# Kernel tuning notes

Hardware: AMD Instinct MI355X
Metric: run time of the kernel (lower is better)

Reference implementation:

```python
import jax, jax.numpy as jnp
import numpy as np

N_HEAD = 16
D_MODEL = 1024
D_K = 64
D_V = 64
LN_EPS = 1e-6


def setup_inputs() -> dict:
    key = jax.random.key(0)
    ks = jax.random.split(key, 10)
    B, S = 2, 2048
    scale = 0.02
    return {
        "q": jax.random.normal(ks[0], (B, S, D_MODEL), jnp.float32),
        "k": jax.random.normal(ks[1], (B, S, D_MODEL), jnp.float32),
        "v": jax.random.normal(ks[2], (B, S, D_MODEL), jnp.float32),
        "Wq": jax.random.normal(ks[3], (D_MODEL, N_HEAD * D_K), jnp.float32) * scale,
        "Wk": jax.random.normal(ks[4], (D_MODEL, N_HEAD * D_K), jnp.float32) * scale,
        "Wv": jax.random.normal(ks[5], (D_MODEL, N_HEAD * D_V), jnp.float32) * scale,
        "Wfc": jax.random.normal(ks[6], (N_HEAD * D_V, D_MODEL), jnp.float32) * scale,
        "bfc": jnp.zeros((D_MODEL,), jnp.float32),
        "gamma": jnp.ones((D_MODEL,), jnp.float32),
        "beta": jnp.zeros((D_MODEL,), jnp.float32),
    }


def reference(q, k, v, Wq, Wk, Wv, Wfc, bfc, gamma, beta):
    B, S, _ = q.shape
    residual = q
    # QKV projections, split into heads: [B, S, H, Dh]
    qh = (q @ Wq).reshape(B, S, N_HEAD, D_K)
    kh = (k @ Wk).reshape(B, S, N_HEAD, D_K)
    vh = (v @ Wv).reshape(B, S, N_HEAD, D_V)
    # scaled dot-product attention (explicit score matrix, as in source)
    temperature = jnp.asarray(D_K, qh.dtype) ** 0.5
    attn = jnp.einsum("bqhd,bkhd->bhqk", qh, kh) / temperature
    attn = jax.nn.softmax(attn, axis=-1)
    out = jnp.einsum("bhqk,bkhd->bqhd", attn, vh).reshape(B, S, N_HEAD * D_V)
    # output projection (dropout is identity in eval mode)
    out = out @ Wfc + bfc
    # residual + layernorm (eps=1e-6)
    x = out + residual
    mu = jnp.mean(x, axis=-1, keepdims=True)
    var = jnp.mean(jnp.square(x - mu), axis=-1, keepdims=True)
    return (x - mu) / jnp.sqrt(var + LN_EPS) * gamma + beta
```

## Files before the change

kernel.cpp:

```cpp
#include <hip/hip_runtime.h>

typedef float f32x4 __attribute__((ext_vector_type(4)));
typedef short short8 __attribute__((ext_vector_type(8)));
typedef short short4v __attribute__((ext_vector_type(4)));
typedef unsigned short ushort_t;

#define D_MODEL 1024
#define N_HEAD 16
#define SEQ 2048
#define BATCH 2
#define M_TOK 4096
#define HD 1024
#define NT 32
#define QSCALE_L2E 0.1803368801111f

__device__ __forceinline__ ushort_t f2bf(float f) {
    union { float f; unsigned int u; } x; x.f = f;
    unsigned int r = x.u + 0x7fffu + ((x.u >> 16) & 1u);
    return (ushort_t)(r >> 16);
}
__device__ __forceinline__ ushort_t f2bf_fast(float f) {
    union { float f; unsigned int u; } x; x.f = f;
    return (ushort_t)((x.u + 0x8000u) >> 16);
}

__device__ __forceinline__ void async_copy16(const ushort_t* gptr, ushort_t* lptr) {
    __builtin_amdgcn_global_load_lds(
        (const __attribute__((address_space(1))) unsigned int*)gptr,
        (__attribute__((address_space(3))) unsigned int*)lptr, 16, 0, 0);
}

__global__ __launch_bounds__(256) void transpose_cast4(const float* __restrict__ w0,
                                                       const float* __restrict__ w1,
                                                       const float* __restrict__ w2,
                                                       const float* __restrict__ w3,
                                                       ushort_t* __restrict__ o0,
                                                       ushort_t* __restrict__ o1,
                                                       ushort_t* __restrict__ o2,
                                                       ushort_t* __restrict__ o3) {
    const int R = D_MODEL, C = D_MODEL;
    int z = blockIdx.z;
    const float* in = (z == 0) ? w0 : (z == 1) ? w1 : (z == 2) ? w2 : w3;
    ushort_t* out = (z == 0) ? o0 : (z == 1) ? o1 : (z == 2) ? o2 : o3;
    __shared__ ushort_t t[32][33];
    int bc = blockIdx.x * 32, br = blockIdx.y * 32;
    for (int i = threadIdx.y; i < 32; i += 8)
        t[i][threadIdx.x] = f2bf(in[(size_t)(br + i) * C + bc + threadIdx.x]);
    __syncthreads();
    for (int i = threadIdx.y; i < 32; i += 8)
        out[(size_t)(bc + i) * R + br + threadIdx.x] = t[threadIdx.x][i];
}

__global__ __launch_bounds__(256) void cast_bf16_3(const float* __restrict__ q,
                                                   const float* __restrict__ k,
                                                   const float* __restrict__ v,
                                                   ushort_t* __restrict__ qo,
                                                   ushort_t* __restrict__ ko,
                                                   ushort_t* __restrict__ vo) {
    int z = blockIdx.z;
    const float* s = (z == 0) ? q : (z == 1) ? k : v;
    ushort_t* d = (z == 0) ? qo : (z == 1) ? ko : vo;
    size_t i = ((size_t)blockIdx.x * 256 + threadIdx.x) * 8;
    float4 a = *(const float4*)(s + i);
    float4 b = *(const float4*)(s + i + 4);
    ushort_t tmp[8] = {f2bf(a.x), f2bf(a.y), f2bf(a.z), f2bf(a.w),
                       f2bf(b.x), f2bf(b.y), f2bf(b.z), f2bf(b.w)};
    *(short8*)(d + i) = *(short8*)tmp;
}

__global__ __launch_bounds__(256) void gemm_qkv(const ushort_t* __restrict__ qb,
                                                const ushort_t* __restrict__ kb,
                                                const ushort_t* __restrict__ vb,
                                                const ushort_t* __restrict__ wq,
                                                const ushort_t* __restrict__ wk,
                                                const ushort_t* __restrict__ wv,
                                                ushort_t* __restrict__ Qo,
                                                ushort_t* __restrict__ Ko,
                                                ushort_t* __restrict__ VtO) {
    __shared__ ushort_t As[128 * 32];
    __shared__ ushort_t Bs[128 * 32];
    const int z = blockIdx.z;
    const ushort_t* A = (z == 0) ? qb : (z == 1) ? kb : vb;
    const ushort_t* Bt = (z == 0) ? wq : (z == 1) ? wk : wv;
    const int tid = threadIdx.x;
    const int wave = tid >> 6, lane = tid & 63;
    const int quad = lane >> 4, l16 = lane & 15;
    const int m0 = blockIdx.y * 128, n0 = blockIdx.x * 128;
    const int wm = (wave >> 1) * 64, wn = (wave & 1) * 64;
    const int K = D_MODEL, N = D_MODEL;

    f32x4 acc[4][4];
    for (int i = 0; i < 4; ++i)
        for (int j = 0; j < 4; ++j) acc[i][j] = (f32x4){0.f, 0.f, 0.f, 0.f};

    for (int kk = 0; kk < K; kk += 32) {
        __syncthreads();
        #pragma unroll
        for (int c = 0; c < 2; ++c) {
            int flat = ((wave * 2 + c) * 64 + lane) * 8;
            int r = flat >> 5, col = flat & 31;
            async_copy16(Bt + (size_t)(n0 + r) * K + kk + col, &Bs[(wave * 2 + c) * 512]);
            async_copy16(A + (size_t)(m0 + r) * K + kk + col, &As[(wave * 2 + c) * 512]);
        }
        __syncthreads();
        short8 af[4], bfr[4];
        #pragma unroll
        for (int i = 0; i < 4; ++i)
            af[i] = *(const short8*)&As[(wm + i * 16 + l16) * 32 + quad * 8];
        #pragma unroll
        for (int j = 0; j < 4; ++j)
            bfr[j] = *(const short8*)&Bs[(wn + j * 16 + l16) * 32 + quad * 8];
        #pragma unroll
        for (int i = 0; i < 4; ++i)
            #pragma unroll
            for (int j = 0; j < 4; ++j)
                acc[i][j] = __builtin_amdgcn_mfma_f32_16x16x32_bf16(af[i], bfr[j], acc[i][j], 0, 0, 0);
    }
    if (z == 2) {
        #pragma unroll
        for (int i = 0; i < 4; ++i)
            #pragma unroll
            for (int j = 0; j < 4; ++j) {
                int n = n0 + wn + j * 16 + l16;
                int mBase = m0 + wm + i * 16;
                int quadR = (quad + (n >> 2)) & 3;
                ushort_t tmp[4];
                #pragma unroll
                for (int r = 0; r < 4; ++r) tmp[r] = f2bf(acc[i][j][r]);
                *(short4v*)&VtO[(size_t)n * M_TOK + mBase + quadR * 4] = *(short4v*)tmp;
            }
    } else {
        ushort_t* C = (z == 0) ? Qo : Ko;
        const float scale = (z == 0) ? QSCALE_L2E : 1.0f;
        #pragma unroll
        for (int i = 0; i < 4; ++i)
            #pragma unroll
            for (int j = 0; j < 4; ++j) {
                int n = n0 + wn + j * 16 + l16;
                #pragma unroll
                for (int r = 0; r < 4; ++r) {
                    int m = m0 + wm + i * 16 + quad * 4 + r;
                    C[(size_t)m * N + n] = f2bf(acc[i][j][r] * scale);
                }
            }
    }
}

__global__ __launch_bounds__(256) void gemm_fc(const ushort_t* __restrict__ A,
                                               const ushort_t* __restrict__ Bt,
                                               float* __restrict__ Cf,
                                               const float* __restrict__ bias,
                                               const float* __restrict__ resid) {
    __shared__ ushort_t As[128 * 32];
    __shared__ ushort_t Bs[64 * 32];
    const int tid = threadIdx.x;
    const int wave = tid >> 6, lane = tid & 63;
    const int quad = lane >> 4, l16 = lane & 15;
    const int m0 = blockIdx.y * 128, n0 = blockIdx.x * 64;
    const int K = D_MODEL, N = D_MODEL;

    f32x4 acc[2][4];
    for (int i = 0; i < 2; ++i)
        for (int j = 0; j < 4; ++j) acc[i][j] = (f32x4){0.f, 0.f, 0.f, 0.f};

    for (int kk = 0; kk < K; kk += 32) {
        __syncthreads();
        #pragma unroll
        for (int c = 0; c < 2; ++c) {
            int g = wave * 2 + c;
            int flat = (g * 64 + lane) * 8;
            int r = flat >> 5, col = flat & 31;
            async_copy16(A + (size_t)(m0 + r) * K + kk + col, &As[g * 512]);
        }
        {
            int flat = (wave * 64 + lane) * 8;
            int r = flat >> 5, col = flat & 31;
            async_copy16(Bt + (size_t)(n0 + r) * K + kk + col, &Bs[wave * 512]);
        }
        __syncthreads();
        short8 af[2], bfr[4];
        #pragma unroll
        for (int i = 0; i < 2; ++i)
            af[i] = *(const short8*)&As[(wave * 32 + i * 16 + l16) * 32 + quad * 8];
        #pragma unroll
        for (int j = 0; j < 4; ++j)
            bfr[j] = *(const short8*)&Bs[(j * 16 + l16) * 32 + quad * 8];
        #pragma unroll
        for (int i = 0; i < 2; ++i)
            #pragma unroll
            for (int j = 0; j < 4; ++j)
                acc[i][j] = __builtin_amdgcn_mfma_f32_16x16x32_bf16(af[i], bfr[j], acc[i][j], 0, 0, 0);
    }
    #pragma unroll
    for (int i = 0; i < 2; ++i)
        #pragma unroll
        for (int j = 0; j < 4; ++j) {
            int n = n0 + j * 16 + l16;
            #pragma unroll
            for (int r = 0; r < 4; ++r) {
                int m = m0 + wave * 32 + i * 16 + quad * 4 + r;
                Cf[(size_t)m * N + n] = acc[i][j][r] + bias[n] + resid[(size_t)m * N + n];
            }
        }
}

__global__ __launch_bounds__(256, 3) void attn64(const ushort_t* __restrict__ Qh,
                                                 const ushort_t* __restrict__ Kh,
                                                 const ushort_t* __restrict__ Vt,
                                                 ushort_t* __restrict__ O) {
    __shared__ __align__(16) char smem[34304];
    const int tid = threadIdx.x;
    const int wave = tid >> 6, lane = tid & 63;
    const int quad = lane >> 4, l16 = lane & 15;
    const int b = blockIdx.z, h = blockIdx.y, qt = blockIdx.x;
    const size_t base = (size_t)b * SEQ * HD + h * 64;
    const ushort_t* Qb = Qh + base + (size_t)(qt * 64) * HD;
    const ushort_t* Kb = Kh + base;
    const ushort_t* Vb = Vt + (size_t)(h * 64) * M_TOK + (size_t)b * SEQ;

    ushort_t* Vw = (ushort_t*)smem + wave * 3072;
    float* lsb = (float*)(smem + 33280);

    short8 qf[4][2];
    #pragma unroll
    for (int nt = 0; nt < 4; ++nt)
        #pragma unroll
        for (int s = 0; s < 2; ++s)
            qf[nt][s] = *(const short8*)(Qb + (size_t)(nt * 16 + l16) * HD + s * 32 + quad * 8);

    f32x4 oacc[4][4];
    #pragma unroll
    for (int nt = 0; nt < 4; ++nt)
        #pragma unroll
        for (int dt = 0; dt < 4; ++dt) oacc[nt][dt] = (f32x4){0.f, 0.f, 0.f, 0.f};
    float lsum[4] = {0.f, 0.f, 0.f, 0.f};

    const ushort_t* Kr = Kb + (size_t)(wave * 16 + l16) * HD + quad * 8;
    const ushort_t* Vg = Vb + (size_t)(lane >> 1) * M_TOK + wave * 16 + (lane & 1) * 8;
    ushort_t* VLd = Vw + lane * 8;

    short8 kf0[2], kf1[2];
    #pragma unroll
    for (int s = 0; s < 2; ++s) kf0[s] = *(const short8*)(Kr + s * 32);
    #pragma unroll
    for (int c = 0; c < 2; ++c)
        async_copy16(Vg + (size_t)c * 32 * M_TOK, VLd + c * 512);
    #pragma unroll
    for (int c = 0; c < 2; ++c)
        async_copy16(Vg + (size_t)c * 32 * M_TOK + 64, VLd + 1024 + c * 512);

    ushort_t *vb0 = Vw, *vb1 = Vw + 1024, *vb2 = Vw + 2048;
    const int rot = (l16 >> 2) & 3;

    for (int kt = 0; kt < NT; ++kt) {
        if (kt == NT - 1) __builtin_amdgcn_s_waitcnt(0x0F70);
        else              __builtin_amdgcn_s_waitcnt(0x0F72);

        if (kt + 1 < NT) {
            #pragma unroll
            for (int s = 0; s < 2; ++s)
                kf1[s] = *(const short8*)(Kr + (size_t)(kt + 1) * 64 * HD + s * 32);
        }
        if (kt + 2 < NT) {
            #pragma unroll
            for (int c = 0; c < 2; ++c)
                async_copy16(Vg + (size_t)c * 32 * M_TOK + (kt + 2) * 64, vb2 + lane * 8 + c * 512);
        }

        short4v vf[4];
        #pragma unroll
        for (int dt = 0; dt < 4; ++dt)
            vf[dt] = *(const short4v*)&vb0[(dt * 16 + l16) * 16 + (((quad + rot) & 3) * 4)];

        f32x4 sacc[4];
        #pragma unroll
        for (int nt = 0; nt < 4; ++nt) sacc[nt] = (f32x4){0.f, 0.f, 0.f, 0.f};
        #pragma unroll
        for (int s = 0; s < 2; ++s)
            #pragma unroll
            for (int nt = 0; nt < 4; ++nt)
                sacc[nt] = __builtin_amdgcn_mfma_f32_16x16x32_bf16(kf0[s], qf[nt][s], sacc[nt], 0, 0, 0);

        short4v pf[4];
        #pragma unroll
        for (int nt = 0; nt < 4; ++nt) {
            ushort_t tmp[4];
            #pragma unroll
            for (int i = 0; i < 4; ++i) {
                float pv = __builtin_amdgcn_exp2f(sacc[nt][i]);
                lsum[nt] += pv;
                tmp[i] = f2bf_fast(pv);
            }
            pf[nt] = *(short4v*)tmp;
        }
        #pragma unroll
        for (int nt = 0; nt < 4; ++nt)
            #pragma unroll
            for (int dt = 0; dt < 4; ++dt)
                oacc[nt][dt] = __builtin_amdgcn_mfma_f32_16x16x16bf16_1k(pf[nt], vf[dt], oacc[nt][dt], 0, 0, 0);

        kf0[0] = kf1[0]; kf0[1] = kf1[1];
        ushort_t* t = vb0; vb0 = vb1; vb1 = vb2; vb2 = t;
    }

    #pragma unroll
    for (int nt = 0; nt < 4; ++nt) {
        lsum[nt] += __shfl_xor(lsum[nt], 16, 64);
        lsum[nt] += __shfl_xor(lsum[nt], 32, 64);
    }
    if (quad == 0) {
        #pragma unroll
        for (int nt = 0; nt < 4; ++nt) lsb[wave * 64 + nt * 16 + l16] = lsum[nt];
    }
    __syncthreads();

    float* R0 = (float*)smem;
    float* R1 = R0 + 64 * 65;
    {
        float* R = (wave & 1) ? R1 : R0;
        if (wave < 2) {
            #pragma unroll
            for (int nt = 0; nt < 4; ++nt)
                #pragma unroll
                for (int dt = 0; dt < 4; ++dt)
                    #pragma unroll
                    for (int i = 0; i < 4; ++i)
                        R[(nt * 16 + quad * 4 + i) * 65 + dt * 16 + l16] = oacc[nt][dt][i];
        }
        __syncthreads();
        if (wave >= 2) {
            #pragma unroll
            for (int nt = 0; nt < 4; ++nt)
                #pragma unroll
                for (int dt = 0; dt < 4; ++dt)
                    #pragma unroll
                    for (int i = 0; i < 4; ++i)
                        R[(nt * 16 + quad * 4 + i) * 65 + dt * 16 + l16] += oacc[nt][dt][i];
        }
        __syncthreads();
    }
    float inv[4];
    #pragma unroll
    for (int i = 0; i < 4; ++i) {
        int qrow = wave * 16 + quad * 4 + i;
        float t = lsb[qrow] + lsb[64 + qrow] + lsb[128 + qrow] + lsb[192 + qrow];
        inv[i] = 1.f / t;
    }
    ushort_t* Ob = O + base + (size_t)(qt * 64) * HD;
    #pragma unroll
    for (int i = 0; i < 4; ++i) {
        int qrow = wave * 16 + quad * 4 + i;
        #pragma unroll
        for (int dt = 0; dt < 4; ++dt) {
            int d = dt * 16 + l16;
            float val = R0[qrow * 65 + d] + R1[qrow * 65 + d];
            Ob[(size_t)qrow * HD + d] = f2bf(val * inv[i]);
        }
    }
}

__global__ __launch_bounds__(256) void ln_kernel(float* __restrict__ x,
                                                 const float* __restrict__ gamma,
                                                 const float* __restrict__ beta) {
    const int D = D_MODEL;
    float* xr = x + (size_t)blockIdx.x * D;
    const int tid = threadIdx.x;
    float4 v = *(const float4*)(xr + tid * 4);
    float s = v.x + v.y + v.z + v.w;
    float s2 = v.x * v.x + v.y * v.y + v.z * v.z + v.w * v.w;
    #pragma unroll
    for (int off = 1; off < 64; off <<= 1) {
        s += __shfl_xor(s, off, 64);
        s2 += __shfl_xor(s2, off, 64);
    }
    __shared__ float ws1[4], ws2[4];
    int wave = tid >> 6, lane = tid & 63;
    if (lane == 0) { ws1[wave] = s; ws2[wave] = s2; }
    __syncthreads();
    s = ws1[0] + ws1[1] + ws1[2] + ws1[3];
    s2 = ws2[0] + ws2[1] + ws2[2] + ws2[3];
    float mean = s * (1.f / D);
    float var = s2 * (1.f / D) - mean * mean;
    float rstd = rsqrtf(var + 1e-6f);
    float4 g = *(const float4*)(gamma + tid * 4);
    float4 bt = *(const float4*)(beta + tid * 4);
    float4 o;
    o.x = (v.x - mean) * rstd * g.x + bt.x;
    o.y = (v.y - mean) * rstd * g.y + bt.y;
    o.z = (v.z - mean) * rstd * g.z + bt.z;
    o.w = (v.w - mean) * rstd * g.w + bt.w;
    *(float4*)(xr + tid * 4) = o;
}

extern "C" void kernel_launch(void* const* d_in, const int* in_sizes, int n_in,
                              void* d_out, int out_size, void* d_ws, size_t ws_size,
                              hipStream_t stream) {
    const float* q = (const float*)d_in[0];
    const float* k = (const float*)d_in[1];
    const float* v = (const float*)d_in[2];
    const float* Wq = (const float*)d_in[3];
    const float* Wk = (const float*)d_in[4];
    const float* Wv = (const float*)d_in[5];
    const float* Wfc = (const float*)d_in[6];
    const float* bfc = (const float*)d_in[7];
    const float* gamma = (const float*)d_in[8];
    const float* beta = (const float*)d_in[9];
    float* out = (float*)d_out;

    char* ws = (char*)d_ws;
    const size_t MB = 1u << 20;
    ushort_t* WqT  = (ushort_t*)(ws + 0 * MB);
    ushort_t* WkT  = (ushort_t*)(ws + 2 * MB);
    ushort_t* WvT  = (ushort_t*)(ws + 4 * MB);
    ushort_t* WfcT = (ushort_t*)(ws + 6 * MB);
    ushort_t* qb   = (ushort_t*)(ws + 8 * MB);
    ushort_t* kb   = (ushort_t*)(ws + 16 * MB);
    ushort_t* vb   = (ushort_t*)(ws + 24 * MB);
    ushort_t* Qh   = (ushort_t*)(ws + 32 * MB);
    ushort_t* Kh   = (ushort_t*)(ws + 40 * MB);
    ushort_t* Vt   = (ushort_t*)(ws + 48 * MB);
    ushort_t* Oh   = (ushort_t*)(ws + 8 * MB);

    const int M = M_TOK, D = D_MODEL;
    transpose_cast4<<<dim3(D / 32, D / 32, 4), dim3(32, 8), 0, stream>>>(
        Wq, Wk, Wv, Wfc, WqT, WkT, WvT, WfcT);

    cast_bf16_3<<<dim3(M * D / (256 * 8), 1, 3), 256, 0, stream>>>(q, k, v, qb, kb, vb);

    gemm_qkv<<<dim3(D / 128, M / 128, 3), 256, 0, stream>>>(qb, kb, vb, WqT, WkT, WvT, Qh, Kh, Vt);

    attn64<<<dim3(SEQ / 64, N_HEAD, BATCH), 256, 0, stream>>>(Qh, Kh, Vt, Oh);

    gemm_fc<<<dim3(D / 64, M / 128), 256, 0, stream>>>(Oh, WfcT, out, bfc, q);

    ln_kernel<<<M, 256, 0, stream>>>(out, gamma, beta);
}
```

Baseline: 258.0 us.

## Fuse prep kernels, shrink attention LDS reduction, reorder attention grid

Merges the weight transpose-cast and activation cast kernels into one launch with a 7-slice grid, removing a kernel launch. Changes the attention epilogue to a single LDS buffer accumulated by the four waves in turn, which cuts shared memory use and may allow more resident blocks, at the cost of extra barriers. Reorders the attention grid so head and batch vary fastest, which changes the order blocks are scheduled and how K/V reuse is grouped.

```diff
diff --git a/kernel.cpp b/kernel.cpp
--- a/kernel.cpp
+++ b/kernel.cpp
@@ -30,42 +30,46 @@
         (__attribute__((address_space(3))) unsigned int*)lptr, 16, 0, 0);
 }
 
-__global__ __launch_bounds__(256) void transpose_cast4(const float* __restrict__ w0,
-                                                       const float* __restrict__ w1,
-                                                       const float* __restrict__ w2,
-                                                       const float* __restrict__ w3,
-                                                       ushort_t* __restrict__ o0,
-                                                       ushort_t* __restrict__ o1,
-                                                       ushort_t* __restrict__ o2,
-                                                       ushort_t* __restrict__ o3) {
-    const int R = D_MODEL, C = D_MODEL;
-    int z = blockIdx.z;
-    const float* in = (z == 0) ? w0 : (z == 1) ? w1 : (z == 2) ? w2 : w3;
-    ushort_t* out = (z == 0) ? o0 : (z == 1) ? o1 : (z == 2) ? o2 : o3;
-    __shared__ ushort_t t[32][33];
-    int bc = blockIdx.x * 32, br = blockIdx.y * 32;
-    for (int i = threadIdx.y; i < 32; i += 8)
-        t[i][threadIdx.x] = f2bf(in[(size_t)(br + i) * C + bc + threadIdx.x]);
-    __syncthreads();
-    for (int i = threadIdx.y; i < 32; i += 8)
-        out[(size_t)(bc + i) * R + br + threadIdx.x] = t[threadIdx.x][i];
-}
-
-__global__ __launch_bounds__(256) void cast_bf16_3(const float* __restrict__ q,
-                                                   const float* __restrict__ k,
-                                                   const float* __restrict__ v,
-                                                   ushort_t* __restrict__ qo,
-                                                   ushort_t* __restrict__ ko,
-                                                   ushort_t* __restrict__ vo) {
-    int z = blockIdx.z;
-    const float* s = (z == 0) ? q : (z == 1) ? k : v;
-    ushort_t* d = (z == 0) ? qo : (z == 1) ? ko : vo;
-    size_t i = ((size_t)blockIdx.x * 256 + threadIdx.x) * 8;
-    float4 a = *(const float4*)(s + i);
-    float4 b = *(const float4*)(s + i + 4);
-    ushort_t tmp[8] = {f2bf(a.x), f2bf(a.y), f2bf(a.z), f2bf(a.w),
-                       f2bf(b.x), f2bf(b.y), f2bf(b.z), f2bf(b.w)};
-    *(short8*)(d + i) = *(short8*)tmp;
+__global__ __launch_bounds__(256) void prep_fused(const float* __restrict__ w0,
+                                                  const float* __restrict__ w1,
+                                                  const float* __restrict__ w2,
+                                                  const float* __restrict__ w3,
+                                                  ushort_t* __restrict__ o0,
+                                                  ushort_t* __restrict__ o1,
+                                                  ushort_t* __restrict__ o2,
+                                                  ushort_t* __restrict__ o3,
+                                                  const float* __restrict__ q,
+                                                  const float* __restrict__ k,
+                                                  const float* __restrict__ v,
+                                                  ushort_t* __restrict__ qo,
+                                                  ushort_t* __restrict__ ko,
+                                                  ushort_t* __restrict__ vo) {
+    const int z = blockIdx.z;
+    const int tid = threadIdx.x;
+    const int flat = blockIdx.x + 64 * blockIdx.y;
+    if (z < 4) {
+        if (flat >= 1024) return;
+        const int R = D_MODEL, C = D_MODEL;
+        const float* in = (z == 0) ? w0 : (z == 1) ? w1 : (z == 2) ? w2 : w3;
+        ushort_t* out = (z == 0) ? o0 : (z == 1) ? o1 : (z == 2) ? o2 : o3;
+        __shared__ ushort_t t[32][33];
+        int bc = (flat & 31) * 32, br = (flat >> 5) * 32;
+        int tx = tid & 31, ty = tid >> 5;
+        for (int i = ty; i < 32; i += 8)
+            t[i][tx] = f2bf(in[(size_t)(br + i) * C + bc + tx]);
+        __syncthreads();
+        for (int i = ty; i < 32; i += 8)
+            out[(size_t)(bc + i) * R + br + tx] = t[tx][i];
+    } else {
+        const float* s = (z == 4) ? q : (z == 5) ? k : v;
+        ushort_t* d = (z == 4) ? qo : (z == 5) ? ko : vo;
+        size_t i = ((size_t)flat * 256 + tid) * 8;
+        float4 a = *(const float4*)(s + i);
+        float4 b = *(const float4*)(s + i + 4);
+        ushort_t tmp[8] = {f2bf(a.x), f2bf(a.y), f2bf(a.z), f2bf(a.w),
+                           f2bf(b.x), f2bf(b.y), f2bf(b.z), f2bf(b.w)};
+        *(short8*)(d + i) = *(short8*)tmp;
+    }
 }
 
 __global__ __launch_bounds__(256) void gemm_qkv(const ushort_t* __restrict__ qb,
@@ -208,18 +212,18 @@
                                                  const ushort_t* __restrict__ Kh,
                                                  const ushort_t* __restrict__ Vt,
                                                  ushort_t* __restrict__ O) {
-    __shared__ __align__(16) char smem[34304];
+    __shared__ __align__(16) char smem[25600];
     const int tid = threadIdx.x;
     const int wave = tid >> 6, lane = tid & 63;
     const int quad = lane >> 4, l16 = lane & 15;
-    const int b = blockIdx.z, h = blockIdx.y, qt = blockIdx.x;
+    const int h = blockIdx.x, b = blockIdx.y, qt = blockIdx.z;
     const size_t base = (size_t)b * SEQ * HD + h * 64;
     const ushort_t* Qb = Qh + base + (size_t)(qt * 64) * HD;
     const ushort_t* Kb = Kh + base;
     const ushort_t* Vb = Vt + (size_t)(h * 64) * M_TOK + (size_t)b * SEQ;
 
     ushort_t* Vw = (ushort_t*)smem + wave * 3072;
-    float* lsb = (float*)(smem + 33280);
+    float* lsb = (float*)(smem + 24576);
 
     short8 qf[4][2];
     #pragma unroll
@@ -314,28 +318,20 @@
     }
     __syncthreads();
 
-    float* R0 = (float*)smem;
-    float* R1 = R0 + 64 * 65;
-    {
-        float* R = (wave & 1) ? R1 : R0;
-        if (wave < 2) {
+    float* R = (float*)smem;
+    #pragma unroll
+    for (int w = 0; w < 4; ++w) {
+        if (wave == w) {
             #pragma unroll
             for (int nt = 0; nt < 4; ++nt)
                 #pragma unroll
                 for (int dt = 0; dt < 4; ++dt)
                     #pragma unroll
-                    for (int i = 0; i < 4; ++i)
-                        R[(nt * 16 + quad * 4 + i) * 65 + dt * 16 + l16] = oacc[nt][dt][i];
-        }
-        __syncthreads();
-        if (wave >= 2) {
-            #pragma unroll
-            for (int nt = 0; nt < 4; ++nt)
-                #pragma unroll
-                for (int dt = 0; dt < 4; ++dt)
-                    #pragma unroll
-                    for (int i = 0; i < 4; ++i)
-                        R[(nt * 16 + quad * 4 + i) * 65 + dt * 16 + l16] += oacc[nt][dt][i];
+                    for (int i = 0; i < 4; ++i) {
+                        int idx = (nt * 16 + quad * 4 + i) * 66 + dt * 16 + l16;
+                        if (w == 0) R[idx] = oacc[nt][dt][i];
+                        else        R[idx] += oacc[nt][dt][i];
+                    }
         }
         __syncthreads();
     }
@@ -353,8 +349,7 @@
         #pragma unroll
         for (int dt = 0; dt < 4; ++dt) {
             int d = dt * 16 + l16;
-            float val = R0[qrow * 65 + d] + R1[qrow * 65 + d];
-            Ob[(size_t)qrow * HD + d] = f2bf(val * inv[i]);
+            Ob[(size_t)qrow * HD + d] = f2bf(R[qrow * 66 + d] * inv[i]);
         }
     }
 }
@@ -422,14 +417,12 @@
     ushort_t* Oh   = (ushort_t*)(ws + 8 * MB);
 
     const int M = M_TOK, D = D_MODEL;
-    transpose_cast4<<<dim3(D / 32, D / 32, 4), dim3(32, 8), 0, stream>>>(
-        Wq, Wk, Wv, Wfc, WqT, WkT, WvT, WfcT);
-
-    cast_bf16_3<<<dim3(M * D / (256 * 8), 1, 3), 256, 0, stream>>>(q, k, v, qb, kb, vb);
+    prep_fused<<<dim3(64, 32, 7), 256, 0, stream>>>(
+        Wq, Wk, Wv, Wfc, WqT, WkT, WvT, WfcT, q, k, v, qb, kb, vb);
 
     gemm_qkv<<<dim3(D / 128, M / 128, 3), 256, 0, stream>>>(qb, kb, vb, WqT, WkT, WvT, Qh, Kh, Vt);
 
-    attn64<<<dim3(SEQ / 64, N_HEAD, BATCH), 256, 0, stream>>>(Qh, Kh, Vt, Oh);
+    attn64<<<dim3(N_HEAD, BATCH, SEQ / 64), 256, 0, stream>>>(Qh, Kh, Vt, Oh);
 
     gemm_fc<<<dim3(D / 64, M / 128), 256, 0, stream>>>(Oh, WfcT, out, bfc, q);
 
```

Result: no change. 254.1 us (-1.5%).
